# Performance work log

Hardware: AMD Instinct MI355X
Metric: run time of the kernel (lower is better)

The kernel has to match this reference:

```python
import jax, jax.numpy as jnp
import numpy as np
import math

B, S, D, H, R = 4, 2048, 2048, 16, 16
HD = D // H

def setup_inputs() -> dict:
    key = jax.random.key(0)
    ks = jax.random.split(key, 16)
    x = jax.random.normal(ks[0], (B, S, D), dtype=jnp.float32)
    # causal mask: 1 where attendable, 0 where masked (mask==0 -> -1e9)
    mask = jnp.tril(jnp.ones((S, S), dtype=jnp.int32))[None, None, :, :]
    def lin(k):
        return jax.random.normal(k, (D, D), dtype=jnp.float32) / math.sqrt(D)
    def lora(ka, kb):
        A = jax.random.normal(ka, (R, D), dtype=jnp.float32) / math.sqrt(D)
        Bm = jnp.zeros((D, R), dtype=jnp.float32)  # standard LoRA init: B = 0
        return A, Bm
    Aq, Bq = lora(ks[1], ks[2]); Ak, Bk = lora(ks[3], ks[4])
    Av, Bv = lora(ks[5], ks[6]); Ao, Bo = lora(ks[7], ks[8])
    return {"x": x, "mask": mask,
            "Wq": lin(ks[9]), "Aq": Aq, "Bq": Bq,
            "Wk": lin(ks[10]), "Ak": Ak, "Bk": Bk,
            "Wv": lin(ks[11]), "Av": Av, "Bv": Bv,
            "Wo": lin(ks[12]), "Ao": Ao, "Bo": Bo}

def _lora_linear(x, W, A, Bm):
    # y = x @ W^T + (x @ A^T) @ B^T   (LoRA-augmented linear, no bias)
    return x @ W.T + (x @ A.T) @ Bm.T

def reference(x, mask, Wq, Aq, Bq, Wk, Ak, Bk, Wv, Av, Bv, Wo, Ao, Bo):
    b, s, d = x.shape
    def heads(t):
        return t.reshape(b, s, H, HD).transpose(0, 2, 1, 3)  # [B,H,S,HD]
    Q = heads(_lora_linear(x, Wq, Aq, Bq))
    K = heads(_lora_linear(x, Wk, Ak, Bk))
    V = heads(_lora_linear(x, Wv, Av, Bv))
    attn = jnp.einsum('bhqd,bhkd->bhqk', Q, K) / math.sqrt(HD)
    attn = jnp.where(mask == 0, jnp.float32(-1e9), attn)
    attn = jax.nn.softmax(attn, axis=-1)
    out = jnp.einsum('bhqk,bhkd->bhqd', attn, V)  # [B,H,S,HD]
    out = out.transpose(0, 2, 1, 3).reshape(b, s, d)
    return _lora_linear(out, Wo, Ao, Bo)
```

## Files before the change

### kernel.cpp

```cpp
#include <hip/hip_runtime.h>
#include <hip/hip_bf16.h>
#include <stdint.h>


#define L2E 1.4426950408889634f
#define SMSCALE 0.08838834764831845f
#define NEGBIG -3.0e38f

typedef __attribute__((ext_vector_type(4))) float f32x4;
typedef __attribute__((ext_vector_type(16))) float f32x16;
typedef __attribute__((ext_vector_type(8))) __bf16 bfrag;

#if __has_builtin(__builtin_amdgcn_exp2f)
#define EXP2 __builtin_amdgcn_exp2f
#else
#define EXP2 exp2f
#endif

#define DRAIN_VM                                      \
  do {                                                \
    asm volatile("s_waitcnt vmcnt(0)" ::: "memory");  \
    __builtin_amdgcn_sched_barrier(0);                \
  } while (0)

static __device__ __forceinline__ unsigned short f2bf(float f) {
  union { float f; unsigned u; } v; v.f = f;
  unsigned r = v.u + 0x7FFFu + ((v.u >> 16) & 1u);
  return (unsigned short)(r >> 16);
}

static __device__ __forceinline__ void gload16(const void* g, void* l) {
  __builtin_amdgcn_global_load_lds(
      (const __attribute__((address_space(1))) void*)g,
      (__attribute__((address_space(3))) void*)l, 16, 0, 0);
}

struct F4 {
  const float* W[4];
  const float* A[4];
  const float* Bm[4];
};

__global__ __launch_bounds__(256) void k_prep(F4 f, const float* __restrict__ x,
                                              unsigned short* __restrict__ xbf,
                                              unsigned short* __restrict__ Wall) {
  const int bid = blockIdx.x;
  if (bid < 8192) {
    const size_t i = ((size_t)bid * 256 + threadIdx.x) * 8;
    unsigned short o[8];
#pragma unroll
    for (int j = 0; j < 8; ++j) o[j] = f2bf(x[i + j]);
    *(uint4*)(xbf + i) = *(const uint4*)o;
    return;
  }
  const int y = (bid - 8192) >> 11;
  const int n = (bid - 8192) & 2047;
  const int k0 = threadIdx.x * 8;
  const float* W = f.W[y];
  const float* Aa = f.A[y];
  const float* Bm = f.Bm[y];
  const float* wr = W + (size_t)n * 2048 + k0;
  float acc[8];
#pragma unroll
  for (int j = 0; j < 8; ++j) acc[j] = wr[j];
#pragma unroll 4
  for (int r = 0; r < 16; ++r) {
    float b = Bm[n * 16 + r];
    const float* ar = Aa + (size_t)r * 2048 + k0;
#pragma unroll
    for (int j = 0; j < 8; ++j) acc[j] = fmaf(b, ar[j], acc[j]);
  }
  unsigned short o[8];
#pragma unroll
  for (int j = 0; j < 8; ++j) o[j] = f2bf(acc[j]);
  *(uint4*)(Wall + (((size_t)y * 2048 + n) * 2048) + k0) = *(const uint4*)o;
}

template <int MODE>
__global__ __launch_bounds__(512, 2) void k_gemm2(const unsigned short* __restrict__ A,
                                                  const unsigned short* __restrict__ Bw,
                                                  void* __restrict__ Cout, float scale) {
  __shared__ __align__(16) unsigned char lds[131072];
  unsigned char* Al = lds;
  unsigned char* Bl = lds + 65536;
  const int tid = threadIdx.x, ln = tid & 63;
  const int w = tid >> 6, g = ln >> 4, cc = ln & 15;
  const int wm = w >> 2, wn = w & 3;
  const int bid = blockIdx.x;
  const int wg = (bid & 7) * 32 + (bid >> 3);
  const int m0 = (wg >> 3) * 256, n0 = (wg & 7) * 256;

  int soff[2], sdst[2];
#pragma unroll
  for (int i = 0; i < 2; ++i) {
    int cid = i * 512 + tid, r = cid >> 2, p = cid & 3;
    int sc = p ^ ((r >> 1) & 3);
    soff[i] = r * 2048 + sc * 8;
    sdst[i] = cid * 16;
  }
  int aro[8], bro[4];
#pragma unroll
  for (int fm = 0; fm < 8; ++fm) {
    int r = wm * 128 + fm * 16 + cc;
    aro[fm] = r * 64 + ((g ^ ((r >> 1) & 3)) << 4);
  }
#pragma unroll
  for (int fn = 0; fn < 4; ++fn) {
    int r = wn * 64 + fn * 16 + cc;
    bro[fn] = r * 64 + ((g ^ ((r >> 1) & 3)) << 4);
  }

#define STAGE_A(b, kt, h)                                                   \
  do {                                                                      \
    _Pragma("unroll")                                                       \
    for (int i = 0; i < 2; ++i)                                             \
      gload16(A + (size_t)m0 * 2048 + soff[i] + (kt) + (h) * 32,            \
              Al + (b) * 32768 + (h) * 16384 + sdst[i]);                    \
  } while (0)
#define STAGE_B(b, kt, h)                                                   \
  do {                                                                      \
    _Pragma("unroll")                                                       \
    for (int i = 0; i < 2; ++i)                                             \
      gload16(Bw + (size_t)n0 * 2048 + soff[i] + (kt) + (h) * 32,           \
              Bl + (b) * 32768 + (h) * 16384 + sdst[i]);                    \
  } while (0)

  f32x4 acc[8][4] = {};

  STAGE_A(0, 0, 0); STAGE_B(0, 0, 0);
  STAGE_A(0, 0, 1); STAGE_B(0, 0, 1);
  asm volatile("s_waitcnt vmcnt(4)" ::: "memory");
  __builtin_amdgcn_s_barrier();
  __builtin_amdgcn_sched_barrier(0);

  for (int T = 0; T < 32; ++T) {
    const int buf = T & 1;
    const unsigned char* Ab = Al + buf * 32768;
    const unsigned char* Bb = Bl + buf * 32768;
    const int ktn = (T + 1) * 64;
    const bool pf = (T + 1 < 32);
#pragma unroll
    for (int ks = 0; ks < 2; ++ks) {
      bfrag af[8], bf0[2], bf1[2];
#pragma unroll
      for (int fm = 0; fm < 8; ++fm)
        af[fm] = *(const bfrag*)(Ab + ks * 16384 + aro[fm]);
#pragma unroll
      for (int j = 0; j < 2; ++j)
        bf0[j] = *(const bfrag*)(Bb + ks * 16384 + bro[j]);
      if (pf) STAGE_A(buf ^ 1, ktn, ks);
      __builtin_amdgcn_sched_barrier(0);
      __builtin_amdgcn_s_barrier();
      asm volatile("s_waitcnt lgkmcnt(0)" ::: "memory");
      __builtin_amdgcn_sched_barrier(0);
      __builtin_amdgcn_s_setprio(1);
#pragma unroll
      for (int fm = 0; fm < 8; ++fm)
#pragma unroll
        for (int j = 0; j < 2; ++j)
          acc[fm][j] = __builtin_amdgcn_mfma_f32_16x16x32_bf16(af[fm], bf0[j],
                                                               acc[fm][j], 0, 0, 0);
      __builtin_amdgcn_s_setprio(0);
      __builtin_amdgcn_sched_barrier(0);
      __builtin_amdgcn_s_barrier();
#pragma unroll
      for (int j = 0; j < 2; ++j)
        bf1[j] = *(const bfrag*)(Bb + ks * 16384 + bro[2 + j]);
      if (pf) STAGE_B(buf ^ 1, ktn, ks);
      __builtin_amdgcn_sched_barrier(0);
      __builtin_amdgcn_s_barrier();
      asm volatile("s_waitcnt lgkmcnt(0)" ::: "memory");
      __builtin_amdgcn_sched_barrier(0);
      __builtin_amdgcn_s_setprio(1);
#pragma unroll
      for (int fm = 0; fm < 8; ++fm)
#pragma unroll
        for (int j = 0; j < 2; ++j)
          acc[fm][2 + j] = __builtin_amdgcn_mfma_f32_16x16x32_bf16(af[fm], bf1[j],
                                                                   acc[fm][2 + j], 0, 0, 0);
      __builtin_amdgcn_s_setprio(0);
      __builtin_amdgcn_sched_barrier(0);
      if (T < 31) asm volatile("s_waitcnt vmcnt(4)" ::: "memory");
      else if (ks == 0) asm volatile("s_waitcnt vmcnt(0)" ::: "memory");
      __builtin_amdgcn_sched_barrier(0);
      __builtin_amdgcn_s_barrier();
    }
  }
#undef STAGE_A
#undef STAGE_B

#pragma unroll
  for (int fm = 0; fm < 8; ++fm)
#pragma unroll
    for (int fn = 0; fn < 4; ++fn)
#pragma unroll
      for (int r = 0; r < 4; ++r) {
        int row = m0 + wm * 128 + fm * 16 + g * 4 + r;
        int col = n0 + wn * 64 + fn * 16 + cc;
        float v = acc[fm][fn][r];
        if (MODE == 0) {
          int b = row >> 11, s = row & 2047, h = col >> 7, hd = col & 127;
          ((unsigned short*)Cout)[(((size_t)b * 16 + h) * 2048 + s) * 128 + hd] =
              f2bf(v * scale);
        } else if (MODE == 2) {
          int b = row >> 11, s = row & 2047, h = col >> 7, hd = col & 127;
          ((unsigned short*)Cout)[(((size_t)b * 16 + h) * 128 + hd) * 2048 + s] =
              f2bf(v);
        } else {
          ((float*)Cout)[(size_t)row * 2048 + col] = v;
        }
      }
}

__global__ __launch_bounds__(512) void k_attn(const unsigned short* __restrict__ Q,
                                              const unsigned short* __restrict__ K,
                                              const unsigned short* __restrict__ Vt,
                                              unsigned short* __restrict__ O,
                                              int* __restrict__ ctr) {
  __shared__ __align__(16) unsigned char lds[65536];
  __shared__ int s_item;
  const int tid = threadIdx.x;
  const int ln = tid & 63, w = tid >> 6;
  const int l31 = ln & 31, hi = ln >> 5;
  const int rk = l31 & 15;

  for (;;) {
    if (tid == 0) s_item = atomicAdd(ctr, 1);
    __syncthreads();
    const int item = s_item;
    if (item >= 512) return;
    const int qb = 7 - (item >> 6);
    const int bh = item & 63;
    const int q0 = qb * 256;
    const size_t base = (size_t)bh * 2048 * 128;
    const unsigned short* Qb = Q + base;
    const unsigned short* Kb = K + base;
    const unsigned short* Vb = Vt + base;

    const int qw0 = q0 + w * 32;
    const int qg = qw0 + l31;

    bfrag qf[8];
#pragma unroll
    for (int dc = 0; dc < 8; ++dc)
      qf[dc] = *(const bfrag*)(Qb + (size_t)qg * 128 + dc * 16 + hi * 8);

    f32x16 o[4] = {};
    float m_r = NEGBIG, l_r = 0.f;

    const int nt = q0 / 64 + 4;

    auto stage = [&](int buf, int k0) {
      unsigned char* Kt = lds + buf * 32768;
      unsigned char* Vl = Kt + 16384;
#pragma unroll
      for (int i = 0; i < 2; ++i) {
        int cid = i * 512 + tid;
        int row = cid >> 4, p = cid & 15, sc = p ^ (row & 15);
        gload16(Kb + (size_t)(k0 + row) * 128 + sc * 8, Kt + cid * 16);
      }
#pragma unroll
      for (int i = 0; i < 2; ++i) {
        int cid = i * 512 + tid;
        int row = cid >> 4, p = cid & 15, sc = p ^ (row & 15);
        int d = (sc >> 3) * 64 + row;
        gload16(Vb + (size_t)d * 2048 + k0 + (sc & 7) * 8, Vl + cid * 16);
      }
    };

    stage(0, 0);
    DRAIN_VM;
    __syncthreads();
    int buf = 0;

    for (int t = 0; t < nt; ++t) {
      const int k0 = t * 64;
      if (t + 1 < nt) stage(buf ^ 1, k0 + 64);

      if (k0 <= qw0 + 31) {
        const unsigned char* Kt = lds + buf * 32768;
        const unsigned char* Vl = Kt + 16384;

        f32x16 s0 = {}, s1 = {};
#pragma unroll
        for (int dc = 0; dc < 8; ++dc) {
          int c = dc * 2 + hi;
          bfrag ka = *(const bfrag*)(Kt + (size_t)l31 * 256 + ((c ^ rk) << 4));
          bfrag kb2 = *(const bfrag*)(Kt + (size_t)(32 + l31) * 256 + ((c ^ rk) << 4));
          s0 = __builtin_amdgcn_mfma_f32_32x32x16_bf16(ka, qf[dc], s0, 0, 0, 0);
          s1 = __builtin_amdgcn_mfma_f32_32x32x16_bf16(kb2, qf[dc], s1, 0, 0, 0);
        }

        if (k0 + 63 > qw0) {
#pragma unroll
          for (int r = 0; r < 16; ++r) {
            int ko = (r & 3) + 8 * (r >> 2) + 4 * hi;
            if (k0 + ko > qg) s0[r] = NEGBIG;
            if (k0 + 32 + ko > qg) s1[r] = NEGBIG;
          }
        }

        float pmax = s0[0];
#pragma unroll
        for (int r = 1; r < 16; ++r) pmax = fmaxf(pmax, s0[r]);
#pragma unroll
        for (int r = 0; r < 16; ++r) pmax = fmaxf(pmax, s1[r]);
        pmax = fmaxf(pmax, __shfl_xor(pmax, 32));

        if (!__all(pmax - m_r <= 12.f)) {
          float mn = fmaxf(m_r, pmax);
          float al = EXP2(m_r - mn);
          l_r *= al;
#pragma unroll
          for (int db = 0; db < 4; ++db)
#pragma unroll
            for (int r = 0; r < 16; ++r) o[db][r] *= al;
          m_r = mn;
        }

        unsigned qd0[8], qd1[8];
        float rs = 0.f;
#pragma unroll
        for (int s = 0; s < 4; ++s) {
          float p0 = EXP2(s0[4 * s + 0] - m_r), p1 = EXP2(s0[4 * s + 1] - m_r);
          float p2 = EXP2(s0[4 * s + 2] - m_r), p3 = EXP2(s0[4 * s + 3] - m_r);
          rs += (p0 + p1) + (p2 + p3);
          qd0[2 * s] = (unsigned)f2bf(p0) | ((unsigned)f2bf(p1) << 16);
          qd0[2 * s + 1] = (unsigned)f2bf(p2) | ((unsigned)f2bf(p3) << 16);
        }
#pragma unroll
        for (int s = 0; s < 4; ++s) {
          float p0 = EXP2(s1[4 * s + 0] - m_r), p1 = EXP2(s1[4 * s + 1] - m_r);
          float p2 = EXP2(s1[4 * s + 2] - m_r), p3 = EXP2(s1[4 * s + 3] - m_r);
          rs += (p0 + p1) + (p2 + p3);
          qd1[2 * s] = (unsigned)f2bf(p0) | ((unsigned)f2bf(p1) << 16);
          qd1[2 * s + 1] = (unsigned)f2bf(p2) | ((unsigned)f2bf(p3) << 16);
        }
        rs += __shfl_xor(rs, 32);
        l_r += rs;

#define PVSTEP(QD, B0, KC)                                                    \
  do {                                                                        \
    unsigned e0 = QD[B0], e1 = QD[B0 + 1], x0 = QD[B0 + 2], x1 = QD[B0 + 3];  \
    unsigned kp0 = hi ? x0 : e0, kp1 = hi ? x1 : e1;                          \
    unsigned sd0 = hi ? e0 : x0, sd1 = hi ? e1 : x1;                          \
    unsigned rc0 = (unsigned)__shfl_xor((int)sd0, 32);                        \
    unsigned rc1 = (unsigned)__shfl_xor((int)sd1, 32);                        \
    unsigned pw[4];                                                           \
    pw[0] = hi ? rc0 : kp0; pw[1] = hi ? rc1 : kp1;                           \
    pw[2] = hi ? kp0 : rc0; pw[3] = hi ? kp1 : rc1;                           \
    bfrag pf = *(bfrag*)pw;                                                   \
    _Pragma("unroll")                                                         \
    for (int db = 0; db < 4; ++db) {                                          \
      int c = (db >> 1) * 8 + KC * 2 + hi;                                    \
      bfrag vf = *(const bfrag*)(Vl + (size_t)((db & 1) * 32 + l31) * 256 +   \
                                 ((c ^ rk) << 4));                            \
      o[db] = __builtin_amdgcn_mfma_f32_32x32x16_bf16(vf, pf, o[db], 0, 0, 0);\
    }                                                                         \
  } while (0)

        PVSTEP(qd0, 0, 0);
        PVSTEP(qd0, 4, 1);
        PVSTEP(qd1, 0, 2);
        PVSTEP(qd1, 4, 3);
#undef PVSTEP
      }
      DRAIN_VM;
      __syncthreads();
      buf ^= 1;
    }

    float invl = 1.0f / l_r;
    const int b_ = bh >> 4, h_ = bh & 15;
#pragma unroll
    for (int ph = 0; ph < 2; ++ph) {
      if ((w >> 2) == ph) {
        unsigned char* ep = lds + (w & 3) * 8704;
#pragma unroll
        for (int db = 0; db < 4; ++db)
#pragma unroll
          for (int s = 0; s < 4; ++s) {
            int d0 = db * 32 + 8 * s + 4 * hi;
            float v0 = o[db][4 * s] * invl, v1 = o[db][4 * s + 1] * invl;
            float v2 = o[db][4 * s + 2] * invl, v3 = o[db][4 * s + 3] * invl;
            uint2 pw;
            pw.x = (unsigned)f2bf(v0) | ((unsigned)f2bf(v1) << 16);
            pw.y = (unsigned)f2bf(v2) | ((unsigned)f2bf(v3) << 16);
            *(uint2*)(ep + l31 * 272 + d0 * 2) = pw;
          }
      }
      __syncthreads();
      if ((w >> 2) == ph) {
        const unsigned char* ep = lds + (w & 3) * 8704;
#pragma unroll
        for (int i = 0; i < 8; ++i) {
          int cid = i * 64 + ln;
          int q = cid >> 4, ch = cid & 15;
          uint4 val = *(const uint4*)(ep + q * 272 + ch * 16);
          *(uint4*)(O + ((size_t)(b_ * 2048 + q0 + w * 32 + q)) * 2048 +
                    h_ * 128 + ch * 8) = val;
        }
      }
      __syncthreads();
    }
  }
}

extern "C" void kernel_launch(void* const* d_in, const int* in_sizes, int n_in,
                              void* d_out, int out_size, void* d_ws, size_t ws_size,
                              hipStream_t stream) {
  (void)in_sizes; (void)n_in; (void)out_size; (void)ws_size;
  const float* x  = (const float*)d_in[0];

  char* ws = (char*)d_ws;
  unsigned short* xbf  = (unsigned short*)ws;
  unsigned short* Wall = (unsigned short*)(ws + (size_t)33554432);
  unsigned short* Qb   = (unsigned short*)(ws + (size_t)67108864);
  unsigned short* Kb   = Qb + 16777216;
  unsigned short* Vtb  = Kb + 16777216;
  unsigned short* AO   = xbf;
  int* ctr = (int*)(ws + (size_t)167772160);

  F4 f;
  f.W[0] = (const float*)d_in[2];  f.A[0] = (const float*)d_in[3];  f.Bm[0] = (const float*)d_in[4];
  f.W[1] = (const float*)d_in[5];  f.A[1] = (const float*)d_in[6];  f.Bm[1] = (const float*)d_in[7];
  f.W[2] = (const float*)d_in[8];  f.A[2] = (const float*)d_in[9];  f.Bm[2] = (const float*)d_in[10];
  f.W[3] = (const float*)d_in[11]; f.A[3] = (const float*)d_in[12]; f.Bm[3] = (const float*)d_in[13];

  hipMemsetAsync(ctr, 0, 4, stream);
  k_prep<<<16384, 256, 0, stream>>>(f, x, xbf, Wall);

  k_gemm2<0><<<256, 512, 0, stream>>>(xbf, Wall, Qb, SMSCALE * L2E);
  k_gemm2<0><<<256, 512, 0, stream>>>(xbf, Wall + 4194304, Kb, 1.0f);
  k_gemm2<2><<<256, 512, 0, stream>>>(xbf, Wall + 8388608, Vtb, 1.0f);

  k_attn<<<384, 512, 0, stream>>>(Qb, Kb, Vtb, AO, ctr);

  k_gemm2<1><<<256, 512, 0, stream>>>(AO, Wall + 12582912, d_out, 1.0f);
}
```

Before: 428.3 us.

## Load GEMM B operand directly to registers and drop attention work-queue

The GEMM now stages only the A tile through LDS and loads each wave's B fragments straight from global memory into registers, one k-tile ahead. This halves LDS use and removes the per-half-step barriers and LDS reads for B, at the cost of more redundant global traffic for B across waves and more registers. The attention kernel drops its atomic-counter persistent scheduler and launches one block per work item (512 blocks), which also removes the memset. Heavy causal blocks are still ordered first by block index.

```diff
diff --git a/kernel.cpp b/kernel.cpp
--- a/kernel.cpp
+++ b/kernel.cpp
@@ -77,12 +77,10 @@
 }
 
 template <int MODE>
-__global__ __launch_bounds__(512, 2) void k_gemm2(const unsigned short* __restrict__ A,
+__global__ __launch_bounds__(512, 2) void k_gemm5(const unsigned short* __restrict__ A,
                                                   const unsigned short* __restrict__ Bw,
                                                   void* __restrict__ Cout, float scale) {
-  __shared__ __align__(16) unsigned char lds[131072];
-  unsigned char* Al = lds;
-  unsigned char* Bl = lds + 65536;
+  __shared__ __align__(16) unsigned char lds[65536];
   const int tid = threadIdx.x, ln = tid & 63;
   const int w = tid >> 6, g = ln >> 4, cc = ln & 15;
   const int wm = w >> 2, wn = w & 3;
@@ -98,96 +96,84 @@
     soff[i] = r * 2048 + sc * 8;
     sdst[i] = cid * 16;
   }
-  int aro[8], bro[4];
+  int aro[8];
 #pragma unroll
   for (int fm = 0; fm < 8; ++fm) {
     int r = wm * 128 + fm * 16 + cc;
     aro[fm] = r * 64 + ((g ^ ((r >> 1) & 3)) << 4);
   }
-#pragma unroll
-  for (int fn = 0; fn < 4; ++fn) {
-    int r = wn * 64 + fn * 16 + cc;
-    bro[fn] = r * 64 + ((g ^ ((r >> 1) & 3)) << 4);
-  }
+  const unsigned short* Bg = Bw + (size_t)(n0 + wn * 64 + cc) * 2048 + g * 8;
 
 #define STAGE_A(b, kt, h)                                                   \
   do {                                                                      \
     _Pragma("unroll")                                                       \
     for (int i = 0; i < 2; ++i)                                             \
       gload16(A + (size_t)m0 * 2048 + soff[i] + (kt) + (h) * 32,            \
-              Al + (b) * 32768 + (h) * 16384 + sdst[i]);                    \
+              lds + (b) * 32768 + (h) * 16384 + sdst[i]);                   \
   } while (0)
-#define STAGE_B(b, kt, h)                                                   \
+#define ISSUE_B(kt)                                                         \
   do {                                                                      \
     _Pragma("unroll")                                                       \
-    for (int i = 0; i < 2; ++i)                                             \
-      gload16(Bw + (size_t)n0 * 2048 + soff[i] + (kt) + (h) * 32,           \
-              Bl + (b) * 32768 + (h) * 16384 + sdst[i]);                    \
+    for (int ks = 0; ks < 2; ++ks)                                          \
+      _Pragma("unroll")                                                     \
+      for (int fn = 0; fn < 4; ++fn)                                        \
+        bfr[ks][fn] = *(const bfrag*)(Bg + (size_t)fn * 32768 + (kt) +      \
+                                      ks * 32);                             \
   } while (0)
 
   f32x4 acc[8][4] = {};
-
-  STAGE_A(0, 0, 0); STAGE_B(0, 0, 0);
-  STAGE_A(0, 0, 1); STAGE_B(0, 0, 1);
-  asm volatile("s_waitcnt vmcnt(4)" ::: "memory");
+  bfrag bfr[2][4];
+
+  STAGE_A(0, 0, 0); STAGE_A(0, 0, 1);
+  __builtin_amdgcn_sched_barrier(0);
+  ISSUE_B(0);
+  __builtin_amdgcn_sched_barrier(0);
+  asm volatile("s_waitcnt vmcnt(8)" ::: "memory");
   __builtin_amdgcn_s_barrier();
   __builtin_amdgcn_sched_barrier(0);
 
   for (int T = 0; T < 32; ++T) {
-    const int buf = T & 1;
-    const unsigned char* Ab = Al + buf * 32768;
-    const unsigned char* Bb = Bl + buf * 32768;
-    const int ktn = (T + 1) * 64;
-    const bool pf = (T + 1 < 32);
-#pragma unroll
-    for (int ks = 0; ks < 2; ++ks) {
-      bfrag af[8], bf0[2], bf1[2];
-#pragma unroll
-      for (int fm = 0; fm < 8; ++fm)
-        af[fm] = *(const bfrag*)(Ab + ks * 16384 + aro[fm]);
-#pragma unroll
-      for (int j = 0; j < 2; ++j)
-        bf0[j] = *(const bfrag*)(Bb + ks * 16384 + bro[j]);
-      if (pf) STAGE_A(buf ^ 1, ktn, ks);
+    const unsigned char* Ab = lds + (T & 1) * 32768;
+    bfrag af[8];
+#pragma unroll
+    for (int fm = 0; fm < 8; ++fm)
+      af[fm] = *(const bfrag*)(Ab + aro[fm]);
+    __builtin_amdgcn_sched_barrier(0);
+    __builtin_amdgcn_s_setprio(1);
+#pragma unroll
+    for (int fm = 0; fm < 8; ++fm)
+#pragma unroll
+      for (int fn = 0; fn < 4; ++fn)
+        acc[fm][fn] = __builtin_amdgcn_mfma_f32_16x16x32_bf16(af[fm], bfr[0][fn],
+                                                              acc[fm][fn], 0, 0, 0);
+    __builtin_amdgcn_s_setprio(0);
+#pragma unroll
+    for (int fm = 0; fm < 8; ++fm)
+      af[fm] = *(const bfrag*)(Ab + 16384 + aro[fm]);
+    __builtin_amdgcn_sched_barrier(0);
+    __builtin_amdgcn_s_setprio(1);
+#pragma unroll
+    for (int fm = 0; fm < 8; ++fm)
+#pragma unroll
+      for (int fn = 0; fn < 4; ++fn)
+        acc[fm][fn] = __builtin_amdgcn_mfma_f32_16x16x32_bf16(af[fm], bfr[1][fn],
+                                                              acc[fm][fn], 0, 0, 0);
+    __builtin_amdgcn_s_setprio(0);
+    __builtin_amdgcn_sched_barrier(0);
+    if (T < 31) {
+      const int ktn = (T + 1) * 64;
+      STAGE_A((T & 1) ^ 1, ktn, 0); STAGE_A((T & 1) ^ 1, ktn, 1);
+      __builtin_amdgcn_sched_barrier(0);
+      ISSUE_B(ktn);
+      __builtin_amdgcn_sched_barrier(0);
+      asm volatile("s_waitcnt vmcnt(8)" ::: "memory");
       __builtin_amdgcn_sched_barrier(0);
       __builtin_amdgcn_s_barrier();
-      asm volatile("s_waitcnt lgkmcnt(0)" ::: "memory");
       __builtin_amdgcn_sched_barrier(0);
-      __builtin_amdgcn_s_setprio(1);
-#pragma unroll
-      for (int fm = 0; fm < 8; ++fm)
-#pragma unroll
-        for (int j = 0; j < 2; ++j)
-          acc[fm][j] = __builtin_amdgcn_mfma_f32_16x16x32_bf16(af[fm], bf0[j],
-                                                               acc[fm][j], 0, 0, 0);
-      __builtin_amdgcn_s_setprio(0);
-      __builtin_amdgcn_sched_barrier(0);
-      __builtin_amdgcn_s_barrier();
-#pragma unroll
-      for (int j = 0; j < 2; ++j)
-        bf1[j] = *(const bfrag*)(Bb + ks * 16384 + bro[2 + j]);
-      if (pf) STAGE_B(buf ^ 1, ktn, ks);
-      __builtin_amdgcn_sched_barrier(0);
-      __builtin_amdgcn_s_barrier();
-      asm volatile("s_waitcnt lgkmcnt(0)" ::: "memory");
-      __builtin_amdgcn_sched_barrier(0);
-      __builtin_amdgcn_s_setprio(1);
-#pragma unroll
-      for (int fm = 0; fm < 8; ++fm)
-#pragma unroll
-        for (int j = 0; j < 2; ++j)
-          acc[fm][2 + j] = __builtin_amdgcn_mfma_f32_16x16x32_bf16(af[fm], bf1[j],
-                                                                   acc[fm][2 + j], 0, 0, 0);
-      __builtin_amdgcn_s_setprio(0);
-      __builtin_amdgcn_sched_barrier(0);
-      if (T < 31) asm volatile("s_waitcnt vmcnt(4)" ::: "memory");
-      else if (ks == 0) asm volatile("s_waitcnt vmcnt(0)" ::: "memory");
-      __builtin_amdgcn_sched_barrier(0);
-      __builtin_amdgcn_s_barrier();
     }
   }
 #undef STAGE_A
-#undef STAGE_B
+#undef ISSUE_B
 
 #pragma unroll
   for (int fm = 0; fm < 8; ++fm)
@@ -215,129 +201,122 @@
 __global__ __launch_bounds__(512) void k_attn(const unsigned short* __restrict__ Q,
                                               const unsigned short* __restrict__ K,
                                               const unsigned short* __restrict__ Vt,
-                                              unsigned short* __restrict__ O,
-                                              int* __restrict__ ctr) {
+                                              unsigned short* __restrict__ O) {
   __shared__ __align__(16) unsigned char lds[65536];
-  __shared__ int s_item;
   const int tid = threadIdx.x;
   const int ln = tid & 63, w = tid >> 6;
   const int l31 = ln & 31, hi = ln >> 5;
   const int rk = l31 & 15;
-
-  for (;;) {
-    if (tid == 0) s_item = atomicAdd(ctr, 1);
-    __syncthreads();
-    const int item = s_item;
-    if (item >= 512) return;
-    const int qb = 7 - (item >> 6);
-    const int bh = item & 63;
-    const int q0 = qb * 256;
-    const size_t base = (size_t)bh * 2048 * 128;
-    const unsigned short* Qb = Q + base;
-    const unsigned short* Kb = K + base;
-    const unsigned short* Vb = Vt + base;
-
-    const int qw0 = q0 + w * 32;
-    const int qg = qw0 + l31;
-
-    bfrag qf[8];
-#pragma unroll
-    for (int dc = 0; dc < 8; ++dc)
-      qf[dc] = *(const bfrag*)(Qb + (size_t)qg * 128 + dc * 16 + hi * 8);
-
-    f32x16 o[4] = {};
-    float m_r = NEGBIG, l_r = 0.f;
-
-    const int nt = q0 / 64 + 4;
-
-    auto stage = [&](int buf, int k0) {
-      unsigned char* Kt = lds + buf * 32768;
-      unsigned char* Vl = Kt + 16384;
-#pragma unroll
-      for (int i = 0; i < 2; ++i) {
-        int cid = i * 512 + tid;
-        int row = cid >> 4, p = cid & 15, sc = p ^ (row & 15);
-        gload16(Kb + (size_t)(k0 + row) * 128 + sc * 8, Kt + cid * 16);
-      }
-#pragma unroll
-      for (int i = 0; i < 2; ++i) {
-        int cid = i * 512 + tid;
-        int row = cid >> 4, p = cid & 15, sc = p ^ (row & 15);
-        int d = (sc >> 3) * 64 + row;
-        gload16(Vb + (size_t)d * 2048 + k0 + (sc & 7) * 8, Vl + cid * 16);
-      }
-    };
-
-    stage(0, 0);
-    DRAIN_VM;
-    __syncthreads();
-    int buf = 0;
-
-    for (int t = 0; t < nt; ++t) {
-      const int k0 = t * 64;
-      if (t + 1 < nt) stage(buf ^ 1, k0 + 64);
-
-      if (k0 <= qw0 + 31) {
-        const unsigned char* Kt = lds + buf * 32768;
-        const unsigned char* Vl = Kt + 16384;
-
-        f32x16 s0 = {}, s1 = {};
-#pragma unroll
-        for (int dc = 0; dc < 8; ++dc) {
-          int c = dc * 2 + hi;
-          bfrag ka = *(const bfrag*)(Kt + (size_t)l31 * 256 + ((c ^ rk) << 4));
-          bfrag kb2 = *(const bfrag*)(Kt + (size_t)(32 + l31) * 256 + ((c ^ rk) << 4));
-          s0 = __builtin_amdgcn_mfma_f32_32x32x16_bf16(ka, qf[dc], s0, 0, 0, 0);
-          s1 = __builtin_amdgcn_mfma_f32_32x32x16_bf16(kb2, qf[dc], s1, 0, 0, 0);
+  const int bx = blockIdx.x;
+  const int qb = 7 - (bx >> 6);
+  const int bh = bx & 63;
+  const int q0 = qb * 256;
+  const size_t base = (size_t)bh * 2048 * 128;
+  const unsigned short* Qb = Q + base;
+  const unsigned short* Kb = K + base;
+  const unsigned short* Vb = Vt + base;
+
+  const int qw0 = q0 + w * 32;
+  const int qg = qw0 + l31;
+
+  bfrag qf[8];
+#pragma unroll
+  for (int dc = 0; dc < 8; ++dc)
+    qf[dc] = *(const bfrag*)(Qb + (size_t)qg * 128 + dc * 16 + hi * 8);
+
+  f32x16 o[4] = {};
+  float m_r = NEGBIG, l_r = 0.f;
+
+  const int nt = q0 / 64 + 4;
+
+  auto stage = [&](int buf, int k0) {
+    unsigned char* Kt = lds + buf * 32768;
+    unsigned char* Vl = Kt + 16384;
+#pragma unroll
+    for (int i = 0; i < 2; ++i) {
+      int cid = i * 512 + tid;
+      int row = cid >> 4, p = cid & 15, sc = p ^ (row & 15);
+      gload16(Kb + (size_t)(k0 + row) * 128 + sc * 8, Kt + cid * 16);
+    }
+#pragma unroll
+    for (int i = 0; i < 2; ++i) {
+      int cid = i * 512 + tid;
+      int row = cid >> 4, p = cid & 15, sc = p ^ (row & 15);
+      int d = (sc >> 3) * 64 + row;
+      gload16(Vb + (size_t)d * 2048 + k0 + (sc & 7) * 8, Vl + cid * 16);
+    }
+  };
+
+  stage(0, 0);
+  DRAIN_VM;
+  __syncthreads();
+  int buf = 0;
+
+  for (int t = 0; t < nt; ++t) {
+    const int k0 = t * 64;
+    if (t + 1 < nt) stage(buf ^ 1, k0 + 64);
+
+    if (k0 <= qw0 + 31) {
+      const unsigned char* Kt = lds + buf * 32768;
+      const unsigned char* Vl = Kt + 16384;
+
+      f32x16 s0 = {}, s1 = {};
+#pragma unroll
+      for (int dc = 0; dc < 8; ++dc) {
+        int c = dc * 2 + hi;
+        bfrag ka = *(const bfrag*)(Kt + (size_t)l31 * 256 + ((c ^ rk) << 4));
+        bfrag kb2 = *(const bfrag*)(Kt + (size_t)(32 + l31) * 256 + ((c ^ rk) << 4));
+        s0 = __builtin_amdgcn_mfma_f32_32x32x16_bf16(ka, qf[dc], s0, 0, 0, 0);
+        s1 = __builtin_amdgcn_mfma_f32_32x32x16_bf16(kb2, qf[dc], s1, 0, 0, 0);
+      }
+
+      if (k0 + 63 > qw0) {
+#pragma unroll
+        for (int r = 0; r < 16; ++r) {
+          int ko = (r & 3) + 8 * (r >> 2) + 4 * hi;
+          if (k0 + ko > qg) s0[r] = NEGBIG;
+          if (k0 + 32 + ko > qg) s1[r] = NEGBIG;
         }
-
-        if (k0 + 63 > qw0) {
-#pragma unroll
-          for (int r = 0; r < 16; ++r) {
-            int ko = (r & 3) + 8 * (r >> 2) + 4 * hi;
-            if (k0 + ko > qg) s0[r] = NEGBIG;
-            if (k0 + 32 + ko > qg) s1[r] = NEGBIG;
-          }
-        }
-
-        float pmax = s0[0];
-#pragma unroll
-        for (int r = 1; r < 16; ++r) pmax = fmaxf(pmax, s0[r]);
-#pragma unroll
-        for (int r = 0; r < 16; ++r) pmax = fmaxf(pmax, s1[r]);
-        pmax = fmaxf(pmax, __shfl_xor(pmax, 32));
-
-        if (!__all(pmax - m_r <= 12.f)) {
-          float mn = fmaxf(m_r, pmax);
-          float al = EXP2(m_r - mn);
-          l_r *= al;
-#pragma unroll
-          for (int db = 0; db < 4; ++db)
-#pragma unroll
-            for (int r = 0; r < 16; ++r) o[db][r] *= al;
-          m_r = mn;
-        }
-
-        unsigned qd0[8], qd1[8];
-        float rs = 0.f;
-#pragma unroll
-        for (int s = 0; s < 4; ++s) {
-          float p0 = EXP2(s0[4 * s + 0] - m_r), p1 = EXP2(s0[4 * s + 1] - m_r);
-          float p2 = EXP2(s0[4 * s + 2] - m_r), p3 = EXP2(s0[4 * s + 3] - m_r);
-          rs += (p0 + p1) + (p2 + p3);
-          qd0[2 * s] = (unsigned)f2bf(p0) | ((unsigned)f2bf(p1) << 16);
-          qd0[2 * s + 1] = (unsigned)f2bf(p2) | ((unsigned)f2bf(p3) << 16);
-        }
-#pragma unroll
-        for (int s = 0; s < 4; ++s) {
-          float p0 = EXP2(s1[4 * s + 0] - m_r), p1 = EXP2(s1[4 * s + 1] - m_r);
-          float p2 = EXP2(s1[4 * s + 2] - m_r), p3 = EXP2(s1[4 * s + 3] - m_r);
-          rs += (p0 + p1) + (p2 + p3);
-          qd1[2 * s] = (unsigned)f2bf(p0) | ((unsigned)f2bf(p1) << 16);
-          qd1[2 * s + 1] = (unsigned)f2bf(p2) | ((unsigned)f2bf(p3) << 16);
-        }
-        rs += __shfl_xor(rs, 32);
-        l_r += rs;
+      }
+
+      float pmax = s0[0];
+#pragma unroll
+      for (int r = 1; r < 16; ++r) pmax = fmaxf(pmax, s0[r]);
+#pragma unroll
+      for (int r = 0; r < 16; ++r) pmax = fmaxf(pmax, s1[r]);
+      pmax = fmaxf(pmax, __shfl_xor(pmax, 32));
+
+      if (!__all(pmax - m_r <= 12.f)) {
+        float mn = fmaxf(m_r, pmax);
+        float al = EXP2(m_r - mn);
+        l_r *= al;
+#pragma unroll
+        for (int db = 0; db < 4; ++db)
+#pragma unroll
+          for (int r = 0; r < 16; ++r) o[db][r] *= al;
+        m_r = mn;
+      }
+
+      unsigned qd0[8], qd1[8];
+      float rs = 0.f;
+#pragma unroll
+      for (int s = 0; s < 4; ++s) {
+        float p0 = EXP2(s0[4 * s + 0] - m_r), p1 = EXP2(s0[4 * s + 1] - m_r);
+        float p2 = EXP2(s0[4 * s + 2] - m_r), p3 = EXP2(s0[4 * s + 3] - m_r);
+        rs += (p0 + p1) + (p2 + p3);
+        qd0[2 * s] = (unsigned)f2bf(p0) | ((unsigned)f2bf(p1) << 16);
+        qd0[2 * s + 1] = (unsigned)f2bf(p2) | ((unsigned)f2bf(p3) << 16);
+      }
+#pragma unroll
+      for (int s = 0; s < 4; ++s) {
+        float p0 = EXP2(s1[4 * s + 0] - m_r), p1 = EXP2(s1[4 * s + 1] - m_r);
+        float p2 = EXP2(s1[4 * s + 2] - m_r), p3 = EXP2(s1[4 * s + 3] - m_r);
+        rs += (p0 + p1) + (p2 + p3);
+        qd1[2 * s] = (unsigned)f2bf(p0) | ((unsigned)f2bf(p1) << 16);
+        qd1[2 * s + 1] = (unsigned)f2bf(p2) | ((unsigned)f2bf(p3) << 16);
+      }
+      rs += __shfl_xor(rs, 32);
+      l_r += rs;
 
 #define PVSTEP(QD, B0, KC)                                                    \
   do {                                                                        \
@@ -359,50 +338,49 @@
     }                                                                         \
   } while (0)
 
-        PVSTEP(qd0, 0, 0);
-        PVSTEP(qd0, 4, 1);
-        PVSTEP(qd1, 0, 2);
-        PVSTEP(qd1, 4, 3);
+      PVSTEP(qd0, 0, 0);
+      PVSTEP(qd0, 4, 1);
+      PVSTEP(qd1, 0, 2);
+      PVSTEP(qd1, 4, 3);
 #undef PVSTEP
-      }
-      DRAIN_VM;
-      __syncthreads();
-      buf ^= 1;
-    }
-
-    float invl = 1.0f / l_r;
-    const int b_ = bh >> 4, h_ = bh & 15;
-#pragma unroll
-    for (int ph = 0; ph < 2; ++ph) {
-      if ((w >> 2) == ph) {
-        unsigned char* ep = lds + (w & 3) * 8704;
-#pragma unroll
-        for (int db = 0; db < 4; ++db)
-#pragma unroll
-          for (int s = 0; s < 4; ++s) {
-            int d0 = db * 32 + 8 * s + 4 * hi;
-            float v0 = o[db][4 * s] * invl, v1 = o[db][4 * s + 1] * invl;
-            float v2 = o[db][4 * s + 2] * invl, v3 = o[db][4 * s + 3] * invl;
-            uint2 pw;
-            pw.x = (unsigned)f2bf(v0) | ((unsigned)f2bf(v1) << 16);
-            pw.y = (unsigned)f2bf(v2) | ((unsigned)f2bf(v3) << 16);
-            *(uint2*)(ep + l31 * 272 + d0 * 2) = pw;
-          }
-      }
-      __syncthreads();
-      if ((w >> 2) == ph) {
-        const unsigned char* ep = lds + (w & 3) * 8704;
-#pragma unroll
-        for (int i = 0; i < 8; ++i) {
-          int cid = i * 64 + ln;
-          int q = cid >> 4, ch = cid & 15;
-          uint4 val = *(const uint4*)(ep + q * 272 + ch * 16);
-          *(uint4*)(O + ((size_t)(b_ * 2048 + q0 + w * 32 + q)) * 2048 +
-                    h_ * 128 + ch * 8) = val;
+    }
+    DRAIN_VM;
+    __syncthreads();
+    buf ^= 1;
+  }
+
+  float invl = 1.0f / l_r;
+  const int b_ = bh >> 4, h_ = bh & 15;
+#pragma unroll
+  for (int ph = 0; ph < 2; ++ph) {
+    if ((w >> 2) == ph) {
+      unsigned char* ep = lds + (w & 3) * 8704;
+#pragma unroll
+      for (int db = 0; db < 4; ++db)
+#pragma unroll
+        for (int s = 0; s < 4; ++s) {
+          int d0 = db * 32 + 8 * s + 4 * hi;
+          float v0 = o[db][4 * s] * invl, v1 = o[db][4 * s + 1] * invl;
+          float v2 = o[db][4 * s + 2] * invl, v3 = o[db][4 * s + 3] * invl;
+          uint2 pw;
+          pw.x = (unsigned)f2bf(v0) | ((unsigned)f2bf(v1) << 16);
+          pw.y = (unsigned)f2bf(v2) | ((unsigned)f2bf(v3) << 16);
+          *(uint2*)(ep + l31 * 272 + d0 * 2) = pw;
         }
-      }
-      __syncthreads();
-    }
+    }
+    __syncthreads();
+    if ((w >> 2) == ph) {
+      const unsigned char* ep = lds + (w & 3) * 8704;
+#pragma unroll
+      for (int i = 0; i < 8; ++i) {
+        int cid = i * 64 + ln;
+        int q = cid >> 4, ch = cid & 15;
+        uint4 val = *(const uint4*)(ep + q * 272 + ch * 16);
+        *(uint4*)(O + ((size_t)(b_ * 2048 + q0 + w * 32 + q)) * 2048 +
+                  h_ * 128 + ch * 8) = val;
+      }
+    }
+    __syncthreads();
   }
 }
 
@@ -419,7 +397,6 @@
   unsigned short* Kb   = Qb + 16777216;
   unsigned short* Vtb  = Kb + 16777216;
   unsigned short* AO   = xbf;
-  int* ctr = (int*)(ws + (size_t)167772160);
 
   F4 f;
   f.W[0] = (const float*)d_in[2];  f.A[0] = (const float*)d_in[3];  f.Bm[0] = (const float*)d_in[4];
@@ -427,14 +404,13 @@
   f.W[2] = (const float*)d_in[8];  f.A[2] = (const float*)d_in[9];  f.Bm[2] = (const float*)d_in[10];
   f.W[3] = (const float*)d_in[11]; f.A[3] = (const float*)d_in[12]; f.Bm[3] = (const float*)d_in[13];
 
-  hipMemsetAsync(ctr, 0, 4, stream);
   k_prep<<<16384, 256, 0, stream>>>(f, x, xbf, Wall);
 
-  k_gemm2<0><<<256, 512, 0, stream>>>(xbf, Wall, Qb, SMSCALE * L2E);
-  k_gemm2<0><<<256, 512, 0, stream>>>(xbf, Wall + 4194304, Kb, 1.0f);
-  k_gemm2<2><<<256, 512, 0, stream>>>(xbf, Wall + 8388608, Vtb, 1.0f);
-
-  k_attn<<<384, 512, 0, stream>>>(Qb, Kb, Vtb, AO, ctr);
-
-  k_gemm2<1><<<256, 512, 0, stream>>>(AO, Wall + 12582912, d_out, 1.0f);
-}
+  k_gemm5<0><<<256, 512, 0, stream>>>(xbf, Wall, Qb, SMSCALE * L2E);
+  k_gemm5<0><<<256, 512, 0, stream>>>(xbf, Wall + 4194304, Kb, 1.0f);
+  k_gemm5<2><<<256, 512, 0, stream>>>(xbf, Wall + 8388608, Vtb, 1.0f);
+
+  k_attn<<<512, 512, 0, stream>>>(Qb, Kb, Vtb, AO);
+
+  k_gemm5<1><<<256, 512, 0, stream>>>(AO, Wall + 12582912, d_out, 1.0f);
+}
```

After: 497.3 us. 1.16x slower.

## Merge QKV GEMMs into one launch, drop persistent attention scheduler, use packed bf16 cvt

Applied to the files above, without the earlier changes.

The three separate Q/K/V projection GEMM launches become one 768-block launch, where each block picks its weight segment and output layout from its block index. The attention kernel no longer uses a persistent atomic work-queue loop. It launches one block per (q-block, head) item in heaviest-first order, which also removes the counter memset. Softmax probabilities and outputs are converted with the hardware v_cvt_pk_bf16_f32 instruction instead of manual rounding. These changes cut launch and tail overhead and ALU work, but the attention blocks are now scheduled by hardware rather than dynamically balanced.

```diff
diff --git a/kernel.cpp b/kernel.cpp
--- a/kernel.cpp
+++ b/kernel.cpp
@@ -27,6 +27,12 @@
   union { float f; unsigned u; } v; v.f = f;
   unsigned r = v.u + 0x7FFFu + ((v.u >> 16) & 1u);
   return (unsigned short)(r >> 16);
+}
+
+static __device__ __forceinline__ unsigned cvtpk(float lo, float hi) {
+  unsigned r;
+  asm("v_cvt_pk_bf16_f32 %0, %1, %2" : "=v"(r) : "v"(lo), "v"(hi));
+  return r;
 }
 
 static __device__ __forceinline__ void gload16(const void* g, void* l) {
@@ -86,7 +92,10 @@
   const int tid = threadIdx.x, ln = tid & 63;
   const int w = tid >> 6, g = ln >> 4, cc = ln & 15;
   const int wm = w >> 2, wn = w & 3;
-  const int bid = blockIdx.x;
+  const int bx = blockIdx.x;
+  const int seg = (MODE == 3) ? (bx >> 8) : 1;
+  const int bid = (MODE == 3) ? (bx & 255) : bx;
+  if (MODE == 3) Bw += (size_t)seg * 4194304;
   const int wg = (bid & 7) * 32 + (bid >> 3);
   const int m0 = (wg >> 3) * 256, n0 = (wg & 7) * 256;
 
@@ -189,6 +198,7 @@
 #undef STAGE_A
 #undef STAGE_B
 
+  const float sc = (MODE == 3 && seg == 0) ? scale : 1.0f;
 #pragma unroll
   for (int fm = 0; fm < 8; ++fm)
 #pragma unroll
@@ -198,14 +208,13 @@
         int row = m0 + wm * 128 + fm * 16 + g * 4 + r;
         int col = n0 + wn * 64 + fn * 16 + cc;
         float v = acc[fm][fn][r];
-        if (MODE == 0) {
+        if (MODE == 3) {
           int b = row >> 11, s = row & 2047, h = col >> 7, hd = col & 127;
-          ((unsigned short*)Cout)[(((size_t)b * 16 + h) * 2048 + s) * 128 + hd] =
-              f2bf(v * scale);
-        } else if (MODE == 2) {
-          int b = row >> 11, s = row & 2047, h = col >> 7, hd = col & 127;
-          ((unsigned short*)Cout)[(((size_t)b * 16 + h) * 128 + hd) * 2048 + s] =
-              f2bf(v);
+          unsigned short* D = (unsigned short*)Cout + (size_t)seg * 16777216;
+          if (seg < 2)
+            D[(((size_t)b * 16 + h) * 2048 + s) * 128 + hd] = f2bf(v * sc);
+          else
+            D[(((size_t)b * 16 + h) * 128 + hd) * 2048 + s] = f2bf(v);
         } else {
           ((float*)Cout)[(size_t)row * 2048 + col] = v;
         }
@@ -215,129 +224,122 @@
 __global__ __launch_bounds__(512) void k_attn(const unsigned short* __restrict__ Q,
                                               const unsigned short* __restrict__ K,
                                               const unsigned short* __restrict__ Vt,
-                                              unsigned short* __restrict__ O,
-                                              int* __restrict__ ctr) {
+                                              unsigned short* __restrict__ O) {
   __shared__ __align__(16) unsigned char lds[65536];
-  __shared__ int s_item;
   const int tid = threadIdx.x;
   const int ln = tid & 63, w = tid >> 6;
   const int l31 = ln & 31, hi = ln >> 5;
   const int rk = l31 & 15;
-
-  for (;;) {
-    if (tid == 0) s_item = atomicAdd(ctr, 1);
-    __syncthreads();
-    const int item = s_item;
-    if (item >= 512) return;
-    const int qb = 7 - (item >> 6);
-    const int bh = item & 63;
-    const int q0 = qb * 256;
-    const size_t base = (size_t)bh * 2048 * 128;
-    const unsigned short* Qb = Q + base;
-    const unsigned short* Kb = K + base;
-    const unsigned short* Vb = Vt + base;
-
-    const int qw0 = q0 + w * 32;
-    const int qg = qw0 + l31;
-
-    bfrag qf[8];
-#pragma unroll
-    for (int dc = 0; dc < 8; ++dc)
-      qf[dc] = *(const bfrag*)(Qb + (size_t)qg * 128 + dc * 16 + hi * 8);
-
-    f32x16 o[4] = {};
-    float m_r = NEGBIG, l_r = 0.f;
-
-    const int nt = q0 / 64 + 4;
-
-    auto stage = [&](int buf, int k0) {
-      unsigned char* Kt = lds + buf * 32768;
-      unsigned char* Vl = Kt + 16384;
-#pragma unroll
-      for (int i = 0; i < 2; ++i) {
-        int cid = i * 512 + tid;
-        int row = cid >> 4, p = cid & 15, sc = p ^ (row & 15);
-        gload16(Kb + (size_t)(k0 + row) * 128 + sc * 8, Kt + cid * 16);
-      }
-#pragma unroll
-      for (int i = 0; i < 2; ++i) {
-        int cid = i * 512 + tid;
-        int row = cid >> 4, p = cid & 15, sc = p ^ (row & 15);
-        int d = (sc >> 3) * 64 + row;
-        gload16(Vb + (size_t)d * 2048 + k0 + (sc & 7) * 8, Vl + cid * 16);
-      }
-    };
-
-    stage(0, 0);
-    DRAIN_VM;
-    __syncthreads();
-    int buf = 0;
-
-    for (int t = 0; t < nt; ++t) {
-      const int k0 = t * 64;
-      if (t + 1 < nt) stage(buf ^ 1, k0 + 64);
-
-      if (k0 <= qw0 + 31) {
-        const unsigned char* Kt = lds + buf * 32768;
-        const unsigned char* Vl = Kt + 16384;
-
-        f32x16 s0 = {}, s1 = {};
-#pragma unroll
-        for (int dc = 0; dc < 8; ++dc) {
-          int c = dc * 2 + hi;
-          bfrag ka = *(const bfrag*)(Kt + (size_t)l31 * 256 + ((c ^ rk) << 4));
-          bfrag kb2 = *(const bfrag*)(Kt + (size_t)(32 + l31) * 256 + ((c ^ rk) << 4));
-          s0 = __builtin_amdgcn_mfma_f32_32x32x16_bf16(ka, qf[dc], s0, 0, 0, 0);
-          s1 = __builtin_amdgcn_mfma_f32_32x32x16_bf16(kb2, qf[dc], s1, 0, 0, 0);
+  const int bx = blockIdx.x;
+  const int qb = 7 - (bx >> 6);
+  const int bh = bx & 63;
+  const int q0 = qb * 256;
+  const size_t base = (size_t)bh * 2048 * 128;
+  const unsigned short* Qb = Q + base;
+  const unsigned short* Kb = K + base;
+  const unsigned short* Vb = Vt + base;
+
+  const int qw0 = q0 + w * 32;
+  const int qg = qw0 + l31;
+
+  bfrag qf[8];
+#pragma unroll
+  for (int dc = 0; dc < 8; ++dc)
+    qf[dc] = *(const bfrag*)(Qb + (size_t)qg * 128 + dc * 16 + hi * 8);
+
+  f32x16 o[4] = {};
+  float m_r = NEGBIG, l_r = 0.f;
+
+  const int nt = q0 / 64 + 4;
+
+  auto stage = [&](int buf, int k0) {
+    unsigned char* Kt = lds + buf * 32768;
+    unsigned char* Vl = Kt + 16384;
+#pragma unroll
+    for (int i = 0; i < 2; ++i) {
+      int cid = i * 512 + tid;
+      int row = cid >> 4, p = cid & 15, sc = p ^ (row & 15);
+      gload16(Kb + (size_t)(k0 + row) * 128 + sc * 8, Kt + cid * 16);
+    }
+#pragma unroll
+    for (int i = 0; i < 2; ++i) {
+      int cid = i * 512 + tid;
+      int row = cid >> 4, p = cid & 15, sc = p ^ (row & 15);
+      int d = (sc >> 3) * 64 + row;
+      gload16(Vb + (size_t)d * 2048 + k0 + (sc & 7) * 8, Vl + cid * 16);
+    }
+  };
+
+  stage(0, 0);
+  DRAIN_VM;
+  __syncthreads();
+  int buf = 0;
+
+  for (int t = 0; t < nt; ++t) {
+    const int k0 = t * 64;
+    if (t + 1 < nt) stage(buf ^ 1, k0 + 64);
+
+    if (k0 <= qw0 + 31) {
+      const unsigned char* Kt = lds + buf * 32768;
+      const unsigned char* Vl = Kt + 16384;
+
+      f32x16 s0 = {}, s1 = {};
+#pragma unroll
+      for (int dc = 0; dc < 8; ++dc) {
+        int c = dc * 2 + hi;
+        bfrag ka = *(const bfrag*)(Kt + (size_t)l31 * 256 + ((c ^ rk) << 4));
+        bfrag kb2 = *(const bfrag*)(Kt + (size_t)(32 + l31) * 256 + ((c ^ rk) << 4));
+        s0 = __builtin_amdgcn_mfma_f32_32x32x16_bf16(ka, qf[dc], s0, 0, 0, 0);
+        s1 = __builtin_amdgcn_mfma_f32_32x32x16_bf16(kb2, qf[dc], s1, 0, 0, 0);
+      }
+
+      if (k0 + 63 > qw0) {
+#pragma unroll
+        for (int r = 0; r < 16; ++r) {
+          int ko = (r & 3) + 8 * (r >> 2) + 4 * hi;
+          if (k0 + ko > qg) s0[r] = NEGBIG;
+          if (k0 + 32 + ko > qg) s1[r] = NEGBIG;
         }
-
-        if (k0 + 63 > qw0) {
-#pragma unroll
-          for (int r = 0; r < 16; ++r) {
-            int ko = (r & 3) + 8 * (r >> 2) + 4 * hi;
-            if (k0 + ko > qg) s0[r] = NEGBIG;
-            if (k0 + 32 + ko > qg) s1[r] = NEGBIG;
-          }
-        }
-
-        float pmax = s0[0];
-#pragma unroll
-        for (int r = 1; r < 16; ++r) pmax = fmaxf(pmax, s0[r]);
-#pragma unroll
-        for (int r = 0; r < 16; ++r) pmax = fmaxf(pmax, s1[r]);
-        pmax = fmaxf(pmax, __shfl_xor(pmax, 32));
-
-        if (!__all(pmax - m_r <= 12.f)) {
-          float mn = fmaxf(m_r, pmax);
-          float al = EXP2(m_r - mn);
-          l_r *= al;
-#pragma unroll
-          for (int db = 0; db < 4; ++db)
-#pragma unroll
-            for (int r = 0; r < 16; ++r) o[db][r] *= al;
-          m_r = mn;
-        }
-
-        unsigned qd0[8], qd1[8];
-        float rs = 0.f;
-#pragma unroll
-        for (int s = 0; s < 4; ++s) {
-          float p0 = EXP2(s0[4 * s + 0] - m_r), p1 = EXP2(s0[4 * s + 1] - m_r);
-          float p2 = EXP2(s0[4 * s + 2] - m_r), p3 = EXP2(s0[4 * s + 3] - m_r);
-          rs += (p0 + p1) + (p2 + p3);
-          qd0[2 * s] = (unsigned)f2bf(p0) | ((unsigned)f2bf(p1) << 16);
-          qd0[2 * s + 1] = (unsigned)f2bf(p2) | ((unsigned)f2bf(p3) << 16);
-        }
-#pragma unroll
-        for (int s = 0; s < 4; ++s) {
-          float p0 = EXP2(s1[4 * s + 0] - m_r), p1 = EXP2(s1[4 * s + 1] - m_r);
-          float p2 = EXP2(s1[4 * s + 2] - m_r), p3 = EXP2(s1[4 * s + 3] - m_r);
-          rs += (p0 + p1) + (p2 + p3);
-          qd1[2 * s] = (unsigned)f2bf(p0) | ((unsigned)f2bf(p1) << 16);
-          qd1[2 * s + 1] = (unsigned)f2bf(p2) | ((unsigned)f2bf(p3) << 16);
-        }
-        rs += __shfl_xor(rs, 32);
-        l_r += rs;
+      }
+
+      float pmax = s0[0];
+#pragma unroll
+      for (int r = 1; r < 16; ++r) pmax = fmaxf(pmax, s0[r]);
+#pragma unroll
+      for (int r = 0; r < 16; ++r) pmax = fmaxf(pmax, s1[r]);
+      pmax = fmaxf(pmax, __shfl_xor(pmax, 32));
+
+      if (!__all(pmax - m_r <= 12.f)) {
+        float mn = fmaxf(m_r, pmax);
+        float al = EXP2(m_r - mn);
+        l_r *= al;
+#pragma unroll
+        for (int db = 0; db < 4; ++db)
+#pragma unroll
+          for (int r = 0; r < 16; ++r) o[db][r] *= al;
+        m_r = mn;
+      }
+
+      unsigned qd0[8], qd1[8];
+      float rs = 0.f;
+#pragma unroll
+      for (int s = 0; s < 4; ++s) {
+        float p0 = EXP2(s0[4 * s + 0] - m_r), p1 = EXP2(s0[4 * s + 1] - m_r);
+        float p2 = EXP2(s0[4 * s + 2] - m_r), p3 = EXP2(s0[4 * s + 3] - m_r);
+        rs += (p0 + p1) + (p2 + p3);
+        qd0[2 * s] = cvtpk(p0, p1);
+        qd0[2 * s + 1] = cvtpk(p2, p3);
+      }
+#pragma unroll
+      for (int s = 0; s < 4; ++s) {
+        float p0 = EXP2(s1[4 * s + 0] - m_r), p1 = EXP2(s1[4 * s + 1] - m_r);
+        float p2 = EXP2(s1[4 * s + 2] - m_r), p3 = EXP2(s1[4 * s + 3] - m_r);
+        rs += (p0 + p1) + (p2 + p3);
+        qd1[2 * s] = cvtpk(p0, p1);
+        qd1[2 * s + 1] = cvtpk(p2, p3);
+      }
+      rs += __shfl_xor(rs, 32);
+      l_r += rs;
 
 #define PVSTEP(QD, B0, KC)                                                    \
   do {                                                                        \
@@ -359,50 +361,49 @@
     }                                                                         \
   } while (0)
 
-        PVSTEP(qd0, 0, 0);
-        PVSTEP(qd0, 4, 1);
-        PVSTEP(qd1, 0, 2);
-        PVSTEP(qd1, 4, 3);
+      PVSTEP(qd0, 0, 0);
+      PVSTEP(qd0, 4, 1);
+      PVSTEP(qd1, 0, 2);
+      PVSTEP(qd1, 4, 3);
 #undef PVSTEP
-      }
-      DRAIN_VM;
-      __syncthreads();
-      buf ^= 1;
-    }
-
-    float invl = 1.0f / l_r;
-    const int b_ = bh >> 4, h_ = bh & 15;
-#pragma unroll
-    for (int ph = 0; ph < 2; ++ph) {
-      if ((w >> 2) == ph) {
-        unsigned char* ep = lds + (w & 3) * 8704;
-#pragma unroll
-        for (int db = 0; db < 4; ++db)
-#pragma unroll
-          for (int s = 0; s < 4; ++s) {
-            int d0 = db * 32 + 8 * s + 4 * hi;
-            float v0 = o[db][4 * s] * invl, v1 = o[db][4 * s + 1] * invl;
-            float v2 = o[db][4 * s + 2] * invl, v3 = o[db][4 * s + 3] * invl;
-            uint2 pw;
-            pw.x = (unsigned)f2bf(v0) | ((unsigned)f2bf(v1) << 16);
-            pw.y = (unsigned)f2bf(v2) | ((unsigned)f2bf(v3) << 16);
-            *(uint2*)(ep + l31 * 272 + d0 * 2) = pw;
-          }
-      }
-      __syncthreads();
-      if ((w >> 2) == ph) {
-        const unsigned char* ep = lds + (w & 3) * 8704;
-#pragma unroll
-        for (int i = 0; i < 8; ++i) {
-          int cid = i * 64 + ln;
-          int q = cid >> 4, ch = cid & 15;
-          uint4 val = *(const uint4*)(ep + q * 272 + ch * 16);
-          *(uint4*)(O + ((size_t)(b_ * 2048 + q0 + w * 32 + q)) * 2048 +
-                    h_ * 128 + ch * 8) = val;
+    }
+    DRAIN_VM;
+    __syncthreads();
+    buf ^= 1;
+  }
+
+  float invl = 1.0f / l_r;
+  const int b_ = bh >> 4, h_ = bh & 15;
+#pragma unroll
+  for (int ph = 0; ph < 2; ++ph) {
+    if ((w >> 2) == ph) {
+      unsigned char* ep = lds + (w & 3) * 8704;
+#pragma unroll
+      for (int db = 0; db < 4; ++db)
+#pragma unroll
+        for (int s = 0; s < 4; ++s) {
+          int d0 = db * 32 + 8 * s + 4 * hi;
+          float v0 = o[db][4 * s] * invl, v1 = o[db][4 * s + 1] * invl;
+          float v2 = o[db][4 * s + 2] * invl, v3 = o[db][4 * s + 3] * invl;
+          uint2 pw;
+          pw.x = cvtpk(v0, v1);
+          pw.y = cvtpk(v2, v3);
+          *(uint2*)(ep + l31 * 272 + d0 * 2) = pw;
         }
-      }
-      __syncthreads();
-    }
+    }
+    __syncthreads();
+    if ((w >> 2) == ph) {
+      const unsigned char* ep = lds + (w & 3) * 8704;
+#pragma unroll
+      for (int i = 0; i < 8; ++i) {
+        int cid = i * 64 + ln;
+        int q = cid >> 4, ch = cid & 15;
+        uint4 val = *(const uint4*)(ep + q * 272 + ch * 16);
+        *(uint4*)(O + ((size_t)(b_ * 2048 + q0 + w * 32 + q)) * 2048 +
+                  h_ * 128 + ch * 8) = val;
+      }
+    }
+    __syncthreads();
   }
 }
 
@@ -416,10 +417,7 @@
   unsigned short* xbf  = (unsigned short*)ws;
   unsigned short* Wall = (unsigned short*)(ws + (size_t)33554432);
   unsigned short* Qb   = (unsigned short*)(ws + (size_t)67108864);
-  unsigned short* Kb   = Qb + 16777216;
-  unsigned short* Vtb  = Kb + 16777216;
   unsigned short* AO   = xbf;
-  int* ctr = (int*)(ws + (size_t)167772160);
 
   F4 f;
   f.W[0] = (const float*)d_in[2];  f.A[0] = (const float*)d_in[3];  f.Bm[0] = (const float*)d_in[4];
@@ -427,14 +425,11 @@
   f.W[2] = (const float*)d_in[8];  f.A[2] = (const float*)d_in[9];  f.Bm[2] = (const float*)d_in[10];
   f.W[3] = (const float*)d_in[11]; f.A[3] = (const float*)d_in[12]; f.Bm[3] = (const float*)d_in[13];
 
-  hipMemsetAsync(ctr, 0, 4, stream);
   k_prep<<<16384, 256, 0, stream>>>(f, x, xbf, Wall);
 
-  k_gemm2<0><<<256, 512, 0, stream>>>(xbf, Wall, Qb, SMSCALE * L2E);
-  k_gemm2<0><<<256, 512, 0, stream>>>(xbf, Wall + 4194304, Kb, 1.0f);
-  k_gemm2<2><<<256, 512, 0, stream>>>(xbf, Wall + 8388608, Vtb, 1.0f);
-
-  k_attn<<<384, 512, 0, stream>>>(Qb, Kb, Vtb, AO, ctr);
+  k_gemm2<3><<<768, 512, 0, stream>>>(xbf, Wall, Qb, SMSCALE * L2E);
+
+  k_attn<<<512, 512, 0, stream>>>(Qb, Qb + 16777216, Qb + 33554432, AO);
 
   k_gemm2<1><<<256, 512, 0, stream>>>(AO, Wall + 12582912, d_out, 1.0f);
 }
```

Measured after the change: 420.5 us. No clear change (-1.8%).
